# Optimization experiments

Measured on AMD Instinct MI355X. Metric: run time of the kernel, lower is better.

The kernel has to match this reference:

```python
import jax, jax.numpy as jnp
import numpy as np

N = 50000    # nodes
E = 800000   # edges
F = 128      # node_feature_dim
H = 128      # GCN hidden
H2 = 64      # fc1 hidden
T = 8        # num_tactics
G = 64       # graphs in batch


def setup_inputs() -> dict:
    key = jax.random.key(0)
    ks = jax.random.split(key, 12)
    s = 0.05
    return {
        "x": jax.random.normal(ks[0], (N, F), jnp.float32),
        "edge_index": jax.random.randint(ks[1], (2, E), 0, N, dtype=jnp.int32),
        "batch": jnp.sort(jax.random.randint(ks[2], (N,), 0, G, dtype=jnp.int32)),
        "W": jax.random.normal(ks[3], (F, H), jnp.float32) * s,
        "b": jax.random.normal(ks[4], (H,), jnp.float32) * s,
        "fc1_w": jax.random.normal(ks[5], (H, H2), jnp.float32) * s,
        "fc1_b": jax.random.normal(ks[6], (H2,), jnp.float32) * s,
        "actor_w": jax.random.normal(ks[7], (H2, T), jnp.float32) * s,
        "actor_b": jax.random.normal(ks[8], (T,), jnp.float32) * s,
        "critic_w": jax.random.normal(ks[9], (H2, 1), jnp.float32) * s,
        "critic_b": jax.random.normal(ks[10], (1,), jnp.float32) * s,
    }


def _gcn_conv(x, edge_index, W, b):
    # PyG GCNConv: add self-loops, symmetric D^-1/2 (A+I) D^-1/2 normalization,
    # linear transform first, then scatter-add aggregation, then bias.
    n = x.shape[0]
    loops = jnp.arange(n, dtype=edge_index.dtype)
    src = jnp.concatenate([edge_index[0], loops])  # message sources (x_j)
    dst = jnp.concatenate([edge_index[1], loops])  # aggregation targets
    deg = jax.ops.segment_sum(jnp.ones_like(dst, jnp.float32), dst, num_segments=N)
    dinv = deg ** -0.5  # deg >= 1 due to self-loops
    norm = dinv[src] * dinv[dst]                   # [E+N]
    h = x @ W                                      # [N, H]
    msgs = h[src] * norm[:, None]                  # [E+N, H]
    return jax.ops.segment_sum(msgs, dst, num_segments=N) + b


def reference(x, edge_index, batch, W, b, fc1_w, fc1_b, actor_w, actor_b, critic_w, critic_b):
    h = jax.nn.relu(_gcn_conv(x, edge_index, W, b))            # [N, H]
    # global_mean_pool over batch index
    sums = jax.ops.segment_sum(h, batch, num_segments=G)       # [G, H]
    cnts = jax.ops.segment_sum(jnp.ones((h.shape[0],), h.dtype), batch, num_segments=G)
    group_state = sums / jnp.maximum(cnts, 1.0)[:, None]
    z = jax.nn.relu(group_state @ fc1_w + fc1_b)               # [G, H2]
    tactic_probs = jax.nn.softmax(z @ actor_w + actor_b, axis=-1)  # [G, T]
    group_value = z @ critic_w + critic_b                      # [G, 1]
    return tactic_probs, group_value
```

## Files before the change

kernel.cpp:

```cpp
#include <hip/hip_runtime.h>
#include <hip/hip_bf16.h>

#define NN 50000
#define EE 800000
#define FF 128
#define HH 128
#define HID2 64
#define TT 8
#define GG 64
#define NB 196
#define NSB 64
#define EPB (EE / NSB)

__device__ inline unsigned short f2bf(float f) {
    union { float f; unsigned u; } v; v.f = f;
    unsigned r = v.u + 0x7fff + ((v.u >> 16) & 1);
    return (unsigned short)(r >> 16);
}

__global__ __launch_bounds__(1024) void kb1(const int* __restrict__ dst,
                                            int* __restrict__ table) {
    __shared__ int cnt[NB];
    int t = threadIdx.x, blk = blockIdx.x;
    for (int i = t; i < NB; i += 1024) cnt[i] = 0;
    __syncthreads();
    int e0 = blk * EPB;
    for (int e = e0 + t; e < e0 + EPB; e += 1024)
        atomicAdd(&cnt[dst[e] >> 8], 1);
    __syncthreads();
    for (int i = t; i < NB; i += 1024) table[blk * NB + i] = cnt[i];
}

__global__ __launch_bounds__(256) void kb2(int* __restrict__ table,
                                           int* __restrict__ bbase) {
    __shared__ int s[256];
    int b = threadIdx.x;
    int tot = 0;
    if (b < NB)
        for (int blk = 0; blk < NSB; blk++) tot += table[blk * NB + b];
    s[b] = (b < NB) ? tot : 0;
    __syncthreads();
    for (int off = 1; off < 256; off <<= 1) {
        int a = s[b];
        int w = (b >= off) ? s[b - off] : 0;
        __syncthreads();
        s[b] = a + w;
        __syncthreads();
    }
    int base = (b == 0) ? 0 : s[b - 1];
    if (b < NB) {
        bbase[b] = base;
        int run = base;
        for (int blk = 0; blk < NSB; blk++) {
            int v = table[blk * NB + b];
            table[blk * NB + b] = run;
            run += v;
        }
    }
    if (b == 0) bbase[NB] = EE;
}

__global__ __launch_bounds__(1024) void kb3(const int* __restrict__ src,
                                            const int* __restrict__ dst,
                                            const int* __restrict__ table,
                                            unsigned* __restrict__ etmp) {
    __shared__ int ofs[NB];
    __shared__ int cur[NB];
    int t = threadIdx.x, blk = blockIdx.x;
    for (int i = t; i < NB; i += 1024) { ofs[i] = table[blk * NB + i]; cur[i] = 0; }
    __syncthreads();
    int e0 = blk * EPB;
    for (int e = e0 + t; e < e0 + EPB; e += 1024) {
        int d = dst[e];
        int b = d >> 8;
        int r = atomicAdd(&cur[b], 1);
        etmp[ofs[b] + r] = ((unsigned)d << 16) | (unsigned)src[e];
    }
}

__global__ __launch_bounds__(256) void kdeg(const unsigned* __restrict__ etmp,
                                            const int* __restrict__ bbase,
                                            int* __restrict__ deg) {
    __shared__ int cnt[256];
    int t = threadIdx.x, b = blockIdx.x;
    cnt[t] = 0;
    __syncthreads();
    int e0 = bbase[b], e1 = bbase[b + 1];
    for (int e = e0 + t; e < e1; e += 256)
        atomicAdd(&cnt[(etmp[e] >> 16) & 255], 1);
    __syncthreads();
    int node = b * 256 + t;
    if (node < NN) deg[node] = cnt[t];
}

__global__ __launch_bounds__(256) void k_rowptr(const int* __restrict__ deg,
                                                const int* __restrict__ bbase,
                                                int* __restrict__ row_ptr,
                                                float* __restrict__ dinv) {
    __shared__ int s[256];
    int t = threadIdx.x, b = blockIdx.x;
    int i = b * 256 + t;
    int v = (i < NN) ? deg[i] : 0;
    s[t] = v;
    __syncthreads();
    for (int off = 1; off < 256; off <<= 1) {
        int a = s[t];
        int w = (t >= off) ? s[t - off] : 0;
        __syncthreads();
        s[t] = a + w;
        __syncthreads();
    }
    int excl = ((t == 0) ? 0 : s[t - 1]) + bbase[b];
    if (i < NN) {
        row_ptr[i] = excl;
        dinv[i] = rsqrtf((float)(v + 1));
        if (i == NN - 1) row_ptr[NN] = excl + v;
    }
}

__global__ __launch_bounds__(256) void k_filll(const unsigned* __restrict__ etmp,
                                               const int* __restrict__ bbase,
                                               const int* __restrict__ row_ptr,
                                               int* __restrict__ srcs) {
    __shared__ int cur[256];
    int t = threadIdx.x, b = blockIdx.x;
    int node = b * 256 + t;
    cur[t] = row_ptr[(node < NN) ? node : NN];
    __syncthreads();
    int e0 = bbase[b], e1 = bbase[b + 1];
    for (int e = e0 + t; e < e1; e += 256) {
        unsigned u = etmp[e];
        int slot = atomicAdd(&cur[(u >> 16) & 255], 1);
        srcs[slot] = (int)(u & 0xffffu);
    }
}

__global__ __launch_bounds__(256) void k_gemm(const float* __restrict__ x,
                                              const float* __restrict__ W,
                                              const float* __restrict__ dinv,
                                              unsigned* __restrict__ hs) {
    __shared__ float xs[64 * 36];
    __shared__ float ws[32 * 132];
    int tid = threadIdx.x;
    int tx = tid & 15, ty = tid >> 4;
    int r0 = blockIdx.x * 64;
    float acc[4][8];
#pragma unroll
    for (int r = 0; r < 4; r++)
#pragma unroll
        for (int c = 0; c < 8; c++) acc[r][c] = 0.f;

    for (int k0 = 0; k0 < 128; k0 += 32) {
        {
            int row = tid >> 2, q = tid & 3;
            int gr = r0 + row;
            float4 a0 = {0, 0, 0, 0}, a1 = {0, 0, 0, 0};
            if (gr < NN) {
                const float4* p = (const float4*)(x + (size_t)gr * 128 + k0 + q * 8);
                a0 = p[0]; a1 = p[1];
            }
            float* dp = &xs[row * 36 + q * 8];
            ((float4*)dp)[0] = a0; ((float4*)dp)[1] = a1;
        }
        {
            int kr = tid >> 3, q = tid & 7;
            const float4* p = (const float4*)(W + (size_t)(k0 + kr) * 128 + q * 16);
            float4 b0 = p[0], b1 = p[1], b2 = p[2], b3 = p[3];
            float* dp = &ws[kr * 132 + q * 16];
            ((float4*)dp)[0] = b0; ((float4*)dp)[1] = b1;
            ((float4*)dp)[2] = b2; ((float4*)dp)[3] = b3;
        }
        __syncthreads();
#pragma unroll
        for (int kk = 0; kk < 32; kk++) {
            float a[4];
#pragma unroll
            for (int r = 0; r < 4; r++) a[r] = xs[(ty * 4 + r) * 36 + kk];
            float4 b0 = *(const float4*)&ws[kk * 132 + tx * 8];
            float4 b1 = *(const float4*)&ws[kk * 132 + tx * 8 + 4];
            float bv[8] = {b0.x, b0.y, b0.z, b0.w, b1.x, b1.y, b1.z, b1.w};
#pragma unroll
            for (int r = 0; r < 4; r++)
#pragma unroll
                for (int c = 0; c < 8; c++)
                    acc[r][c] = fmaf(a[r], bv[c], acc[r][c]);
        }
        __syncthreads();
    }
#pragma unroll
    for (int r = 0; r < 4; r++) {
        int gr = r0 + ty * 4 + r;
        if (gr < NN) {
            float di = dinv[gr];
            unsigned p0 = f2bf(acc[r][0] * di) | ((unsigned)f2bf(acc[r][1] * di) << 16);
            unsigned p1 = f2bf(acc[r][2] * di) | ((unsigned)f2bf(acc[r][3] * di) << 16);
            unsigned p2 = f2bf(acc[r][4] * di) | ((unsigned)f2bf(acc[r][5] * di) << 16);
            unsigned p3 = f2bf(acc[r][6] * di) | ((unsigned)f2bf(acc[r][7] * di) << 16);
            uint4 o = {p0, p1, p2, p3};
            *(uint4*)(hs + (size_t)gr * 64 + tx * 4) = o;
        }
    }
}

__global__ __launch_bounds__(256) void k_aggr(const uint4* __restrict__ hs4,
                                              const int* __restrict__ row_ptr,
                                              const int* __restrict__ srcs,
                                              const float* __restrict__ dinv,
                                              const float* __restrict__ bias,
                                              float* __restrict__ h2) {
    int tid = threadIdx.x;
    int wave = tid >> 6, lane = tid & 63;
    int q = lane >> 4, sub = lane & 15;
    int i = blockIdx.x * 16 + wave * 4 + q;
    float di = dinv[i];
    uint4 su = hs4[(size_t)i * 16 + sub];
    float a0 = __uint_as_float(su.x << 16);
    float a1 = __uint_as_float(su.x & 0xffff0000u);
    float a2 = __uint_as_float(su.y << 16);
    float a3 = __uint_as_float(su.y & 0xffff0000u);
    float a4 = __uint_as_float(su.z << 16);
    float a5 = __uint_as_float(su.z & 0xffff0000u);
    float a6 = __uint_as_float(su.w << 16);
    float a7 = __uint_as_float(su.w & 0xffff0000u);
    int e = row_ptr[i], e1 = row_ptr[i + 1];
    for (; e + 1 < e1; e += 2) {
        int s0 = srcs[e], s1 = srcs[e + 1];
        uint4 u0 = hs4[(size_t)s0 * 16 + sub];
        uint4 u1 = hs4[(size_t)s1 * 16 + sub];
        a0 += __uint_as_float(u0.x << 16);
        a1 += __uint_as_float(u0.x & 0xffff0000u);
        a2 += __uint_as_float(u0.y << 16);
        a3 += __uint_as_float(u0.y & 0xffff0000u);
        a4 += __uint_as_float(u0.z << 16);
        a5 += __uint_as_float(u0.z & 0xffff0000u);
        a6 += __uint_as_float(u0.w << 16);
        a7 += __uint_as_float(u0.w & 0xffff0000u);
        a0 += __uint_as_float(u1.x << 16);
        a1 += __uint_as_float(u1.x & 0xffff0000u);
        a2 += __uint_as_float(u1.y << 16);
        a3 += __uint_as_float(u1.y & 0xffff0000u);
        a4 += __uint_as_float(u1.z << 16);
        a5 += __uint_as_float(u1.z & 0xffff0000u);
        a6 += __uint_as_float(u1.w << 16);
        a7 += __uint_as_float(u1.w & 0xffff0000u);
    }
    if (e < e1) {
        uint4 u0 = hs4[(size_t)srcs[e] * 16 + sub];
        a0 += __uint_as_float(u0.x << 16);
        a1 += __uint_as_float(u0.x & 0xffff0000u);
        a2 += __uint_as_float(u0.y << 16);
        a3 += __uint_as_float(u0.y & 0xffff0000u);
        a4 += __uint_as_float(u0.z << 16);
        a5 += __uint_as_float(u0.z & 0xffff0000u);
        a6 += __uint_as_float(u0.w << 16);
        a7 += __uint_as_float(u0.w & 0xffff0000u);
    }
    const float4* b4 = (const float4*)(bias + sub * 8);
    float4 bb0 = b4[0], bb1 = b4[1];
    float4 r0, r1;
    r0.x = fmaxf(fmaf(a0, di, bb0.x), 0.f);
    r0.y = fmaxf(fmaf(a1, di, bb0.y), 0.f);
    r0.z = fmaxf(fmaf(a2, di, bb0.z), 0.f);
    r0.w = fmaxf(fmaf(a3, di, bb0.w), 0.f);
    r1.x = fmaxf(fmaf(a4, di, bb1.x), 0.f);
    r1.y = fmaxf(fmaf(a5, di, bb1.y), 0.f);
    r1.z = fmaxf(fmaf(a6, di, bb1.z), 0.f);
    r1.w = fmaxf(fmaf(a7, di, bb1.w), 0.f);
    float4* o = (float4*)(h2 + (size_t)i * 128 + sub * 8);
    o[0] = r0; o[1] = r1;
}

__device__ inline int lbound(const int* __restrict__ a, int n, int key) {
    int lo = 0, hi = n;
    while (lo < hi) {
        int mid = (lo + hi) >> 1;
        if (a[mid] < key) lo = mid + 1;
        else hi = mid;
    }
    return lo;
}

__global__ __launch_bounds__(128) void k_pool(const float* __restrict__ h2,
                                              const int* __restrict__ batch,
                                              float* __restrict__ gsum) {
    int g = blockIdx.x >> 4, chunk = blockIdx.x & 15;
    int lo = lbound(batch, NN, g);
    int hi = lbound(batch, NN, g + 1);
    int cnt = hi - lo;
    int per = (cnt + 15) >> 4;
    int rs = lo + chunk * per;
    int re = rs + per;
    if (re > hi) re = hi;
    if (rs >= re) return;
    float s = 0.f;
    int f = threadIdx.x;
    for (int r = rs; r < re; ++r) s += h2[(size_t)r * 128 + f];
    atomicAdd(&gsum[g * 128 + f], s);
}

__global__ __launch_bounds__(64) void k_head(const float* __restrict__ gsum,
                                             const int* __restrict__ batch,
                                             const float* __restrict__ fc1_w,
                                             const float* __restrict__ fc1_b,
                                             const float* __restrict__ actor_w,
                                             const float* __restrict__ actor_b,
                                             const float* __restrict__ critic_w,
                                             const float* __restrict__ critic_b,
                                             float* __restrict__ out) {
    __shared__ float gs[128];
    __shared__ float zs[64];
    __shared__ float ls[8], es[8];
    int g = blockIdx.x, t = threadIdx.x;
    int lo = lbound(batch, NN, g), hi = lbound(batch, NN, g + 1);
    float invc = 1.f / fmaxf((float)(hi - lo), 1.f);
    gs[t] = gsum[g * 128 + t] * invc;
    gs[t + 64] = gsum[g * 128 + 64 + t] * invc;
    __syncthreads();
    float z = fc1_b[t];
    for (int k = 0; k < 128; k++) z = fmaf(gs[k], fc1_w[k * 64 + t], z);
    zs[t] = fmaxf(z, 0.f);
    __syncthreads();
    if (t < 8) {
        float l = actor_b[t];
        for (int k = 0; k < 64; k++) l = fmaf(zs[k], actor_w[k * 8 + t], l);
        ls[t] = l;
    }
    __syncthreads();
    if (t < 8) {
        float m = ls[0];
#pragma unroll
        for (int j = 1; j < 8; j++) m = fmaxf(m, ls[j]);
        es[t] = expf(ls[t] - m);
    }
    __syncthreads();
    if (t < 8) {
        float ssum = 0.f;
#pragma unroll
        for (int j = 0; j < 8; j++) ssum += es[j];
        out[g * 8 + t] = es[t] / ssum;
    }
    if (t == 32) {
        float v = critic_b[0];
        for (int k = 0; k < 64; k++) v = fmaf(zs[k], critic_w[k], v);
        out[GG * TT + g] = v;
    }
}

extern "C" void kernel_launch(void* const* d_in, const int* in_sizes, int n_in,
                              void* d_out, int out_size, void* d_ws, size_t ws_size,
                              hipStream_t stream) {
    const float* x        = (const float*)d_in[0];
    const int*   ei       = (const int*)d_in[1];
    const int*   batch    = (const int*)d_in[2];
    const float* W        = (const float*)d_in[3];
    const float* b        = (const float*)d_in[4];
    const float* fc1_w    = (const float*)d_in[5];
    const float* fc1_b    = (const float*)d_in[6];
    const float* actor_w  = (const float*)d_in[7];
    const float* actor_b  = (const float*)d_in[8];
    const float* critic_w = (const float*)d_in[9];
    const float* critic_b = (const float*)d_in[10];
    float* out = (float*)d_out;

    char* ws = (char*)d_ws;
    size_t off = 0;
    unsigned* hs     = (unsigned*)(ws + off); off += (size_t)NN * 64 * 4;
    float* h2        = (float*)(ws + off);    off += (size_t)NN * HH * 4;
    float* dinv      = (float*)(ws + off);    off += (size_t)NN * 4;
    int*   deg       = (int*)(ws + off);      off += (size_t)NN * 4;
    int*   row_ptr   = (int*)(ws + off);      off += (size_t)(NN + 1) * 4 + 12;
    int*   srcs      = (int*)(ws + off);      off += (size_t)EE * 4;
    unsigned* etmp   = (unsigned*)(ws + off); off += (size_t)EE * 4;
    int*   table     = (int*)(ws + off);      off += (size_t)NSB * NB * 4;
    int*   bbase     = (int*)(ws + off);      off += (size_t)(NB + 1) * 4;
    float* gsum      = (float*)(ws + off);    off += (size_t)GG * HH * 4;

    hipMemsetAsync(gsum, 0, (size_t)GG * HH * 4, stream);

    const int* src = ei;
    const int* dst = ei + EE;

    kb1<<<NSB, 1024, 0, stream>>>(dst, table);
    kb2<<<1, 256, 0, stream>>>(table, bbase);
    kb3<<<NSB, 1024, 0, stream>>>(src, dst, table, etmp);
    kdeg<<<NB, 256, 0, stream>>>(etmp, bbase, deg);
    k_rowptr<<<NB, 256, 0, stream>>>(deg, bbase, row_ptr, dinv);
    k_filll<<<NB, 256, 0, stream>>>(etmp, bbase, row_ptr, srcs);
    k_gemm<<<(NN + 63) / 64, 256, 0, stream>>>(x, W, dinv, hs);
    k_aggr<<<NN / 16, 256, 0, stream>>>((const uint4*)hs, row_ptr, srcs, dinv, b, h2);
    k_pool<<<GG * 16, 128, 0, stream>>>(h2, batch, gsum);
    k_head<<<GG, 64, 0, stream>>>(gsum, batch, fc1_w, fc1_b, actor_w, actor_b,
                                  critic_w, critic_b, out);
}
```

Before: 227.1 us.

## Fuse mean pooling into aggregation and merge CSR build kernels

Fuses the global mean pool into the aggregation kernel by accumulating per-graph partial sums in shared memory and flushing them with global atomics, eliminating the full h2 intermediate buffer and the separate pool kernel. Merges the degree count, row pointer scan and source fill into a single CSR kernel, and rebalances the bucketing kernels to more, smaller blocks. The gather loop is unrolled to four neighbours. The 32KB shared accumulator per block and the extra atomics may reduce occupancy of the gather-bound kernel.

```diff
diff --git a/kernel.cpp b/kernel.cpp
--- a/kernel.cpp
+++ b/kernel.cpp
@@ -9,7 +9,7 @@
 #define TT 8
 #define GG 64
 #define NB 196
-#define NSB 64
+#define NSB 256
 #define EPB (EE / NSB)
 
 __device__ inline unsigned short f2bf(float f) {
@@ -18,17 +18,17 @@
     return (unsigned short)(r >> 16);
 }
 
-__global__ __launch_bounds__(1024) void kb1(const int* __restrict__ dst,
-                                            int* __restrict__ table) {
+__global__ __launch_bounds__(256) void kb1(const int* __restrict__ dst,
+                                           int* __restrict__ table) {
     __shared__ int cnt[NB];
     int t = threadIdx.x, blk = blockIdx.x;
-    for (int i = t; i < NB; i += 1024) cnt[i] = 0;
+    for (int i = t; i < NB; i += 256) cnt[i] = 0;
     __syncthreads();
     int e0 = blk * EPB;
-    for (int e = e0 + t; e < e0 + EPB; e += 1024)
+    for (int e = e0 + t; e < e0 + EPB; e += 256)
         atomicAdd(&cnt[dst[e] >> 8], 1);
     __syncthreads();
-    for (int i = t; i < NB; i += 1024) table[blk * NB + i] = cnt[i];
+    for (int i = t; i < NB; i += 256) table[blk * NB + i] = cnt[i];
 }
 
 __global__ __launch_bounds__(256) void kb2(int* __restrict__ table,
@@ -60,17 +60,17 @@
     if (b == 0) bbase[NB] = EE;
 }
 
-__global__ __launch_bounds__(1024) void kb3(const int* __restrict__ src,
-                                            const int* __restrict__ dst,
-                                            const int* __restrict__ table,
-                                            unsigned* __restrict__ etmp) {
+__global__ __launch_bounds__(256) void kb3(const int* __restrict__ src,
+                                           const int* __restrict__ dst,
+                                           const int* __restrict__ table,
+                                           unsigned* __restrict__ etmp) {
     __shared__ int ofs[NB];
     __shared__ int cur[NB];
     int t = threadIdx.x, blk = blockIdx.x;
-    for (int i = t; i < NB; i += 1024) { ofs[i] = table[blk * NB + i]; cur[i] = 0; }
+    for (int i = t; i < NB; i += 256) { ofs[i] = table[blk * NB + i]; cur[i] = 0; }
     __syncthreads();
     int e0 = blk * EPB;
-    for (int e = e0 + t; e < e0 + EPB; e += 1024) {
+    for (int e = e0 + t; e < e0 + EPB; e += 256) {
         int d = dst[e];
         int b = d >> 8;
         int r = atomicAdd(&cur[b], 1);
@@ -78,31 +78,21 @@
     }
 }
 
-__global__ __launch_bounds__(256) void kdeg(const unsigned* __restrict__ etmp,
-                                            const int* __restrict__ bbase,
-                                            int* __restrict__ deg) {
-    __shared__ int cnt[256];
+__global__ __launch_bounds__(256) void k_csr(const unsigned* __restrict__ etmp,
+                                             const int* __restrict__ bbase,
+                                             int* __restrict__ row_ptr,
+                                             float* __restrict__ dinv,
+                                             int* __restrict__ srcs) {
+    __shared__ int s[256];
+    __shared__ int cur[256];
     int t = threadIdx.x, b = blockIdx.x;
-    cnt[t] = 0;
+    s[t] = 0;
     __syncthreads();
     int e0 = bbase[b], e1 = bbase[b + 1];
     for (int e = e0 + t; e < e1; e += 256)
-        atomicAdd(&cnt[(etmp[e] >> 16) & 255], 1);
-    __syncthreads();
-    int node = b * 256 + t;
-    if (node < NN) deg[node] = cnt[t];
-}
-
-__global__ __launch_bounds__(256) void k_rowptr(const int* __restrict__ deg,
-                                                const int* __restrict__ bbase,
-                                                int* __restrict__ row_ptr,
-                                                float* __restrict__ dinv) {
-    __shared__ int s[256];
-    int t = threadIdx.x, b = blockIdx.x;
-    int i = b * 256 + t;
-    int v = (i < NN) ? deg[i] : 0;
-    s[t] = v;
-    __syncthreads();
+        atomicAdd(&s[(etmp[e] >> 16) & 255], 1);
+    __syncthreads();
+    int v = s[t];
     for (int off = 1; off < 256; off <<= 1) {
         int a = s[t];
         int w = (t >= off) ? s[t - off] : 0;
@@ -110,24 +100,15 @@
         s[t] = a + w;
         __syncthreads();
     }
-    int excl = ((t == 0) ? 0 : s[t - 1]) + bbase[b];
-    if (i < NN) {
-        row_ptr[i] = excl;
-        dinv[i] = rsqrtf((float)(v + 1));
-        if (i == NN - 1) row_ptr[NN] = excl + v;
-    }
-}
-
-__global__ __launch_bounds__(256) void k_filll(const unsigned* __restrict__ etmp,
-                                               const int* __restrict__ bbase,
-                                               const int* __restrict__ row_ptr,
-                                               int* __restrict__ srcs) {
-    __shared__ int cur[256];
-    int t = threadIdx.x, b = blockIdx.x;
+    int excl = s[t] - v + e0;
     int node = b * 256 + t;
-    cur[t] = row_ptr[(node < NN) ? node : NN];
-    __syncthreads();
-    int e0 = bbase[b], e1 = bbase[b + 1];
+    if (node < NN) {
+        row_ptr[node] = excl;
+        dinv[node] = rsqrtf((float)(v + 1));
+    }
+    if (b == NB - 1 && t == 0) row_ptr[NN] = EE;
+    cur[t] = excl;
+    __syncthreads();
     for (int e = e0 + t; e < e1; e += 256) {
         unsigned u = etmp[e];
         int slot = atomicAdd(&cur[(u >> 16) & 255], 1);
@@ -207,67 +188,101 @@
                                               const int* __restrict__ srcs,
                                               const float* __restrict__ dinv,
                                               const float* __restrict__ bias,
-                                              float* __restrict__ h2) {
+                                              const int* __restrict__ batch,
+                                              float* __restrict__ gsum) {
+    __shared__ float gacc[GG * 128];
     int tid = threadIdx.x;
-    int wave = tid >> 6, lane = tid & 63;
-    int q = lane >> 4, sub = lane & 15;
-    int i = blockIdx.x * 16 + wave * 4 + q;
-    float di = dinv[i];
-    uint4 su = hs4[(size_t)i * 16 + sub];
-    float a0 = __uint_as_float(su.x << 16);
-    float a1 = __uint_as_float(su.x & 0xffff0000u);
-    float a2 = __uint_as_float(su.y << 16);
-    float a3 = __uint_as_float(su.y & 0xffff0000u);
-    float a4 = __uint_as_float(su.z << 16);
-    float a5 = __uint_as_float(su.z & 0xffff0000u);
-    float a6 = __uint_as_float(su.w << 16);
-    float a7 = __uint_as_float(su.w & 0xffff0000u);
-    int e = row_ptr[i], e1 = row_ptr[i + 1];
-    for (; e + 1 < e1; e += 2) {
-        int s0 = srcs[e], s1 = srcs[e + 1];
-        uint4 u0 = hs4[(size_t)s0 * 16 + sub];
-        uint4 u1 = hs4[(size_t)s1 * 16 + sub];
-        a0 += __uint_as_float(u0.x << 16);
-        a1 += __uint_as_float(u0.x & 0xffff0000u);
-        a2 += __uint_as_float(u0.y << 16);
-        a3 += __uint_as_float(u0.y & 0xffff0000u);
-        a4 += __uint_as_float(u0.z << 16);
-        a5 += __uint_as_float(u0.z & 0xffff0000u);
-        a6 += __uint_as_float(u0.w << 16);
-        a7 += __uint_as_float(u0.w & 0xffff0000u);
-        a0 += __uint_as_float(u1.x << 16);
-        a1 += __uint_as_float(u1.x & 0xffff0000u);
-        a2 += __uint_as_float(u1.y << 16);
-        a3 += __uint_as_float(u1.y & 0xffff0000u);
-        a4 += __uint_as_float(u1.z << 16);
-        a5 += __uint_as_float(u1.z & 0xffff0000u);
-        a6 += __uint_as_float(u1.w << 16);
-        a7 += __uint_as_float(u1.w & 0xffff0000u);
-    }
-    if (e < e1) {
-        uint4 u0 = hs4[(size_t)srcs[e] * 16 + sub];
-        a0 += __uint_as_float(u0.x << 16);
-        a1 += __uint_as_float(u0.x & 0xffff0000u);
-        a2 += __uint_as_float(u0.y << 16);
-        a3 += __uint_as_float(u0.y & 0xffff0000u);
-        a4 += __uint_as_float(u0.z << 16);
-        a5 += __uint_as_float(u0.z & 0xffff0000u);
-        a6 += __uint_as_float(u0.w << 16);
-        a7 += __uint_as_float(u0.w & 0xffff0000u);
-    }
+    int qid = tid >> 4, sub = tid & 15;
+    int i_base = blockIdx.x * 32;
+    int g_first = batch[i_base];
+    int last = i_base + 31; if (last >= NN) last = NN - 1;
+    int gspan = batch[last] - g_first + 1;
+    for (int idx = tid; idx < gspan * 128; idx += 256) gacc[idx] = 0.f;
+    __syncthreads();
+
     const float4* b4 = (const float4*)(bias + sub * 8);
     float4 bb0 = b4[0], bb1 = b4[1];
-    float4 r0, r1;
-    r0.x = fmaxf(fmaf(a0, di, bb0.x), 0.f);
-    r0.y = fmaxf(fmaf(a1, di, bb0.y), 0.f);
-    r0.z = fmaxf(fmaf(a2, di, bb0.z), 0.f);
-    r0.w = fmaxf(fmaf(a3, di, bb0.w), 0.f);
-    r1.x = fmaxf(fmaf(a4, di, bb1.x), 0.f);
-    r1.y = fmaxf(fmaf(a5, di, bb1.y), 0.f);
-    r1.z = fmaxf(fmaf(a6, di, bb1.z), 0.f);
-    r1.w = fmaxf(fmaf(a7, di, bb1.w), 0.f);
-    float4* o = (float4*)(h2 + (size_t)i * 128 + sub * 8);
-    o[0] = r0; o[1] = r1;
+
+    float racc[8];
+#pragma unroll
+    for (int j = 0; j < 8; j++) racc[j] = 0.f;
+    int cur_lg = -1;
+
+    for (int n = 0; n < 2; n++) {
+        int i = i_base + qid * 2 + n;
+        if (i >= NN) break;
+        int lg = batch[i] - g_first;
+        if (lg != cur_lg) {
+            if (cur_lg >= 0) {
+                float* gp = &gacc[cur_lg * 128 + sub * 8];
+#pragma unroll
+                for (int j = 0; j < 8; j++) atomicAdd(&gp[j], racc[j]);
+#pragma unroll
+                for (int j = 0; j < 8; j++) racc[j] = 0.f;
+            }
+            cur_lg = lg;
+        }
+        float di = dinv[i];
+        uint4 su = hs4[(size_t)i * 16 + sub];
+        float a0 = __uint_as_float(su.x << 16);
+        float a1 = __uint_as_float(su.x & 0xffff0000u);
+        float a2 = __uint_as_float(su.y << 16);
+        float a3 = __uint_as_float(su.y & 0xffff0000u);
+        float a4 = __uint_as_float(su.z << 16);
+        float a5 = __uint_as_float(su.z & 0xffff0000u);
+        float a6 = __uint_as_float(su.w << 16);
+        float a7 = __uint_as_float(su.w & 0xffff0000u);
+        int e = row_ptr[i], e1 = row_ptr[i + 1];
+        for (; e + 3 < e1; e += 4) {
+            int s0 = srcs[e], s1 = srcs[e + 1], s2 = srcs[e + 2], s3 = srcs[e + 3];
+            uint4 u0 = hs4[(size_t)s0 * 16 + sub];
+            uint4 u1 = hs4[(size_t)s1 * 16 + sub];
+            uint4 u2 = hs4[(size_t)s2 * 16 + sub];
+            uint4 u3 = hs4[(size_t)s3 * 16 + sub];
+            a0 += __uint_as_float(u0.x << 16); a1 += __uint_as_float(u0.x & 0xffff0000u);
+            a2 += __uint_as_float(u0.y << 16); a3 += __uint_as_float(u0.y & 0xffff0000u);
+            a4 += __uint_as_float(u0.z << 16); a5 += __uint_as_float(u0.z & 0xffff0000u);
+            a6 += __uint_as_float(u0.w << 16); a7 += __uint_as_float(u0.w & 0xffff0000u);
+            a0 += __uint_as_float(u1.x << 16); a1 += __uint_as_float(u1.x & 0xffff0000u);
+            a2 += __uint_as_float(u1.y << 16); a3 += __uint_as_float(u1.y & 0xffff0000u);
+            a4 += __uint_as_float(u1.z << 16); a5 += __uint_as_float(u1.z & 0xffff0000u);
+            a6 += __uint_as_float(u1.w << 16); a7 += __uint_as_float(u1.w & 0xffff0000u);
+            a0 += __uint_as_float(u2.x << 16); a1 += __uint_as_float(u2.x & 0xffff0000u);
+            a2 += __uint_as_float(u2.y << 16); a3 += __uint_as_float(u2.y & 0xffff0000u);
+            a4 += __uint_as_float(u2.z << 16); a5 += __uint_as_float(u2.z & 0xffff0000u);
+            a6 += __uint_as_float(u2.w << 16); a7 += __uint_as_float(u2.w & 0xffff0000u);
+            a0 += __uint_as_float(u3.x << 16); a1 += __uint_as_float(u3.x & 0xffff0000u);
+            a2 += __uint_as_float(u3.y << 16); a3 += __uint_as_float(u3.y & 0xffff0000u);
+            a4 += __uint_as_float(u3.z << 16); a5 += __uint_as_float(u3.z & 0xffff0000u);
+            a6 += __uint_as_float(u3.w << 16); a7 += __uint_as_float(u3.w & 0xffff0000u);
+        }
+        for (; e < e1; ++e) {
+            uint4 u0 = hs4[(size_t)srcs[e] * 16 + sub];
+            a0 += __uint_as_float(u0.x << 16); a1 += __uint_as_float(u0.x & 0xffff0000u);
+            a2 += __uint_as_float(u0.y << 16); a3 += __uint_as_float(u0.y & 0xffff0000u);
+            a4 += __uint_as_float(u0.z << 16); a5 += __uint_as_float(u0.z & 0xffff0000u);
+            a6 += __uint_as_float(u0.w << 16); a7 += __uint_as_float(u0.w & 0xffff0000u);
+        }
+        racc[0] += fmaxf(fmaf(a0, di, bb0.x), 0.f);
+        racc[1] += fmaxf(fmaf(a1, di, bb0.y), 0.f);
+        racc[2] += fmaxf(fmaf(a2, di, bb0.z), 0.f);
+        racc[3] += fmaxf(fmaf(a3, di, bb0.w), 0.f);
+        racc[4] += fmaxf(fmaf(a4, di, bb1.x), 0.f);
+        racc[5] += fmaxf(fmaf(a5, di, bb1.y), 0.f);
+        racc[6] += fmaxf(fmaf(a6, di, bb1.z), 0.f);
+        racc[7] += fmaxf(fmaf(a7, di, bb1.w), 0.f);
+    }
+    if (cur_lg >= 0) {
+        float* gp = &gacc[cur_lg * 128 + sub * 8];
+#pragma unroll
+        for (int j = 0; j < 8; j++) atomicAdd(&gp[j], racc[j]);
+    }
+    __syncthreads();
+    for (int idx = tid; idx < gspan * 128; idx += 256) {
+        float v = gacc[idx];
+        if (v != 0.f)
+            atomicAdd(&gsum[(g_first + (idx >> 7)) * 128 + (idx & 127)], v);
+    }
 }
 
 __device__ inline int lbound(const int* __restrict__ a, int n, int key) {
@@ -278,24 +293,6 @@
         else hi = mid;
     }
     return lo;
-}
-
-__global__ __launch_bounds__(128) void k_pool(const float* __restrict__ h2,
-                                              const int* __restrict__ batch,
-                                              float* __restrict__ gsum) {
-    int g = blockIdx.x >> 4, chunk = blockIdx.x & 15;
-    int lo = lbound(batch, NN, g);
-    int hi = lbound(batch, NN, g + 1);
-    int cnt = hi - lo;
-    int per = (cnt + 15) >> 4;
-    int rs = lo + chunk * per;
-    int re = rs + per;
-    if (re > hi) re = hi;
-    if (rs >= re) return;
-    float s = 0.f;
-    int f = threadIdx.x;
-    for (int r = rs; r < re; ++r) s += h2[(size_t)r * 128 + f];
-    atomicAdd(&gsum[g * 128 + f], s);
 }
 
 __global__ __launch_bounds__(64) void k_head(const float* __restrict__ gsum,
@@ -365,9 +362,7 @@
     char* ws = (char*)d_ws;
     size_t off = 0;
     unsigned* hs     = (unsigned*)(ws + off); off += (size_t)NN * 64 * 4;
-    float* h2        = (float*)(ws + off);    off += (size_t)NN * HH * 4;
     float* dinv      = (float*)(ws + off);    off += (size_t)NN * 4;
-    int*   deg       = (int*)(ws + off);      off += (size_t)NN * 4;
     int*   row_ptr   = (int*)(ws + off);      off += (size_t)(NN + 1) * 4 + 12;
     int*   srcs      = (int*)(ws + off);      off += (size_t)EE * 4;
     unsigned* etmp   = (unsigned*)(ws + off); off += (size_t)EE * 4;
@@ -380,15 +375,13 @@
     const int* src = ei;
     const int* dst = ei + EE;
 
-    kb1<<<NSB, 1024, 0, stream>>>(dst, table);
+    kb1<<<NSB, 256, 0, stream>>>(dst, table);
     kb2<<<1, 256, 0, stream>>>(table, bbase);
-    kb3<<<NSB, 1024, 0, stream>>>(src, dst, table, etmp);
-    kdeg<<<NB, 256, 0, stream>>>(etmp, bbase, deg);
-    k_rowptr<<<NB, 256, 0, stream>>>(deg, bbase, row_ptr, dinv);
-    k_filll<<<NB, 256, 0, stream>>>(etmp, bbase, row_ptr, srcs);
+    kb3<<<NSB, 256, 0, stream>>>(src, dst, table, etmp);
+    k_csr<<<NB, 256, 0, stream>>>(etmp, bbase, row_ptr, dinv, srcs);
     k_gemm<<<(NN + 63) / 64, 256, 0, stream>>>(x, W, dinv, hs);
-    k_aggr<<<NN / 16, 256, 0, stream>>>((const uint4*)hs, row_ptr, srcs, dinv, b, h2);
-    k_pool<<<GG * 16, 128, 0, stream>>>(h2, batch, gsum);
+    k_aggr<<<(NN + 31) / 32, 256, 0, stream>>>((const uint4*)hs, row_ptr, srcs,
+                                               dinv, b, batch, gsum);
     k_head<<<GG, 64, 0, stream>>>(gsum, batch, fc1_w, fc1_b, actor_w, actor_b,
                                   critic_w, critic_b, out);
 }
```

After: 221.2 us. 2.6% less time.
